# Kernel optimization log

Measured on AMD Instinct MI355X. Metric: run time of the kernel, lower is better.

The kernel has to match this reference:

```python
import jax, jax.numpy as jnp
import numpy as np

PC_RANGE = np.array([-51.2, -51.2, -3.2, 51.2, 51.2, 3.2], dtype=np.float32)
VOXEL = 0.2
T_, Z_, Y_, X_ = 5, 32, 512, 512
N_RAYS = 10000
N_STEPS = 768  # unit-voxel steps, enough to traverse the 512x512 grid diagonally


def setup_inputs() -> dict:
    key = jax.random.key(0)
    k1, k2, k3, k4 = jax.random.split(key, 4)
    grid_feats = jax.random.normal(k1, (1, T_, Z_, Y_, X_), jnp.float32)
    # sensor origins near the ego vehicle (meters)
    output_origin = jax.random.uniform(k2, (1, T_, 3), jnp.float32, -2.0, 2.0)
    # LiDAR endpoints: wide in x/y, shallow in z (meters)
    pts = jax.random.normal(k3, (1, N_RAYS, 3), jnp.float32) * 15.0
    pts = pts.at[..., 2].set(jnp.clip(pts[..., 2] * 0.1, -3.0, 3.0))
    output_tindex = jax.random.randint(k4, (1, N_RAYS), 0, T_, dtype=jnp.int32)
    return {"grid_feats": grid_feats, "output_origin": output_origin,
            "output_points": pts, "output_tindex": output_tindex}


def _render(sigma, origin_v, points_v, tindex):
    """Volumetric ray marching (dvr.render math, fixed-step traversal).
    sigma: [B,T,Z,Y,X] nonneg densities; origin_v/points_v in voxel coords (x,y,z).
    Returns expected termination distance and gt distance per ray (voxel units)."""
    B, T, Z, Y, X = sigma.shape
    tindex = tindex.astype(jnp.int32)
    orig = jnp.take_along_axis(origin_v, tindex[..., None].astype(jnp.int32), axis=1)  # [B,N,3]
    dirv = points_v - orig
    gt_dist = jnp.linalg.norm(dirv, axis=-1)                       # [B,N]
    unit = dirv / jnp.maximum(gt_dist[..., None], 1e-6)
    t = jnp.arange(N_STEPS, dtype=sigma.dtype) + 0.5               # [K] step = 1 voxel
    pos = orig[:, :, None, :] + unit[:, :, None, :] * t[None, None, :, None]  # [B,N,K,3]
    idx = jnp.floor(pos).astype(jnp.int32)
    ix, iy, iz = idx[..., 0], idx[..., 1], idx[..., 2]
    inb = (ix >= 0) & (ix < X) & (iy >= 0) & (iy < Y) & (iz >= 0) & (iz < Z)
    ixc = jnp.clip(ix, 0, X - 1)
    iyc = jnp.clip(iy, 0, Y - 1)
    izc = jnp.clip(iz, 0, Z - 1)
    bidx = jnp.arange(B, dtype=jnp.int32)[:, None, None]
    sig = sigma[bidx, tindex[:, :, None], izc, iyc, ixc]           # [B,N,K]
    tau = jnp.where(inb, sig, 0.0)                                 # dt = 1 voxel
    trans = jnp.exp(-(jnp.cumsum(tau, axis=-1) - tau))             # exclusive transmittance
    w = trans * (1.0 - jnp.exp(-tau))                              # termination prob per step
    pred_dist = jnp.sum(w * t, axis=-1)                            # expected depth [B,N]
    return pred_dist, gt_dist


def reference(grid_feats, output_origin, output_points, output_tindex):
    offset = jnp.asarray(PC_RANGE[:3])
    origin_v = (output_origin - offset) / VOXEL
    points_v = (output_points - offset) / VOXEL
    sigma = jax.nn.relu(grid_feats)
    pred, gt = _render(sigma, origin_v, points_v, output_tindex)
    pred = pred * VOXEL
    gt = gt * VOXEL
    valid = gt >= 0
    count = jnp.maximum(valid.sum(), 1).astype(pred.dtype)
    diff = gt - pred
    l1 = jnp.where(valid, jnp.abs(diff), 0.0).sum() / count
    l2 = jnp.where(valid, diff * diff * 0.5, 0.0).sum() / count
    absrel = jnp.where(valid, jnp.abs(diff) / jnp.maximum(gt, 1e-6), 0.0).sum() / count
    return jnp.stack([l1, l2, absrel])
```

## Files before the change

### kernel.cpp

```cpp
#include <hip/hip_runtime.h>
#include <math.h>

#define T_DIM 5
#define Z_DIM 32
#define Y_DIM 512
#define X_DIM 512
#define N_RAYS 10000
#define N_STEPS 768
#define VOXEL_F 0.2f


__global__ __launch_bounds__(256) void render_rays_kernel(
    const float* __restrict__ grid,
    const float* __restrict__ origin,
    const float* __restrict__ points,
    const int*   __restrict__ tindex,
    float4*      __restrict__ loss4)
{
    const int wid  = (int)((blockIdx.x * blockDim.x + threadIdx.x) >> 6);
    const int lane = (int)(threadIdx.x & 63);
    if (wid >= N_RAYS) return;
    const int ray = wid;

    const int ti = tindex[ray];
    const float ox = (origin[ti * 3 + 0] + 51.2f) * 5.0f;
    const float oy = (origin[ti * 3 + 1] + 51.2f) * 5.0f;
    const float oz = (origin[ti * 3 + 2] + 3.2f) * 5.0f;
    const float px = (points[ray * 3 + 0] + 51.2f) * 5.0f;
    const float py = (points[ray * 3 + 1] + 51.2f) * 5.0f;
    const float pz = (points[ray * 3 + 2] + 3.2f) * 5.0f;

    const float dx = px - ox, dy = py - oy, dz = pz - oz;
    const float gt_vox = sqrtf(dx * dx + dy * dy + dz * dz);
    const float inv = 1.0f / fmaxf(gt_vox, 1e-6f);
    const float ux = dx * inv, uy = dy * inv, uz = dz * inv;

    float thi = 1e30f;
    thi = fminf(thi, fmaxf((0.0f - ox) / ux, ((float)X_DIM - ox) / ux));
    thi = fminf(thi, fmaxf((0.0f - oy) / uy, ((float)Y_DIM - oy) / uy));
    thi = fminf(thi, fmaxf((0.0f - oz) / uz, ((float)Z_DIM - oz) / uz));
    int n_active = (int)ceilf(fminf(thi, 769.0f) - 0.5f);
    n_active = min(N_STEPS, max(0, n_active));
    const int iters = (n_active + 63) >> 6;

    const float* gbase = grid + (size_t)ti * (size_t)(Z_DIM * Y_DIM * X_DIM);

    float lane_acc = 0.0f;
    float ecarry   = 1.0f;

    for (int j = 0; j < iters; ++j) {
        const int step = (j << 6) + lane;
        const float tt = (float)step + 0.5f;
        const int ix = (int)floorf(fmaf(ux, tt, ox));
        const int iy = (int)floorf(fmaf(uy, tt, oy));
        const int iz = (int)floorf(fmaf(uz, tt, oz));
        const bool inb = (ix >= 0) & (ix < X_DIM) & (iy >= 0) & (iy < Y_DIM) &
                         (iz >= 0) & (iz < Z_DIM);
        float tau = 0.0f;
        if ((step < n_active) && inb) {
            tau = fmaxf(gbase[((size_t)iz * Y_DIM + (size_t)iy) * X_DIM + (size_t)ix], 0.0f);
        }

        float scan = tau;
#pragma unroll
        for (int d = 1; d < 64; d <<= 1) {
            const float up = __shfl_up(scan, d, 64);
            if (lane >= d) scan += up;
        }

        const float e_scan = expf(-scan);
        lane_acc += ecarry * (expf(tau - scan) - e_scan) * tt;

        ecarry *= __shfl(e_scan, 63, 64);
        if (ecarry < 1e-7f) break;
    }

#pragma unroll
    for (int d = 32; d >= 1; d >>= 1) lane_acc += __shfl_xor(lane_acc, d, 64);

    if (lane == 0) {
        const float pred_m = lane_acc * VOXEL_F;
        const float gt_m   = gt_vox * VOXEL_F;
        const float diff = gt_m - pred_m;
        const float ad   = fabsf(diff);
        float4 v;
        v.x = ad;
        v.y = 0.5f * diff * diff;
        v.z = ad / fmaxf(gt_m, 1e-6f);
        v.w = 1.0f;
        loss4[wid] = v;
    }
}

__global__ __launch_bounds__(1024) void finalize_kernel(
    const float4* __restrict__ loss4, float* __restrict__ out)
{
    const int tid  = (int)threadIdx.x;
    const int lane = tid & 63;
    const int wv   = tid >> 6;
    float a = 0.0f, b = 0.0f, c = 0.0f, n = 0.0f;
    for (int i = tid; i < N_RAYS; i += 1024) {
        const float4 v = loss4[i];
        a += v.x; b += v.y; c += v.z; n += v.w;
    }
#pragma unroll
    for (int d = 32; d >= 1; d >>= 1) {
        a += __shfl_xor(a, d, 64);
        b += __shfl_xor(b, d, 64);
        c += __shfl_xor(c, d, 64);
        n += __shfl_xor(n, d, 64);
    }
    __shared__ float red[16][4];
    if (lane == 0) { red[wv][0] = a; red[wv][1] = b; red[wv][2] = c; red[wv][3] = n; }
    __syncthreads();
    if (wv == 0 && lane < 16) {
        a = red[lane][0]; b = red[lane][1]; c = red[lane][2]; n = red[lane][3];
#pragma unroll
        for (int d = 8; d >= 1; d >>= 1) {
            a += __shfl_xor(a, d, 64);
            b += __shfl_xor(b, d, 64);
            c += __shfl_xor(c, d, 64);
            n += __shfl_xor(n, d, 64);
        }
        if (lane == 0) {
            const float cnt = fmaxf(n, 1.0f);
            out[0] = a / cnt;
            out[1] = b / cnt;
            out[2] = c / cnt;
        }
    }
}

extern "C" void kernel_launch(void* const* d_in, const int* in_sizes, int n_in,
                              void* d_out, int out_size, void* d_ws, size_t ws_size,
                              hipStream_t stream) {
    const float* grid    = (const float*)d_in[0];
    const float* origin  = (const float*)d_in[1];
    const float* points  = (const float*)d_in[2];
    const int*   tindex  = (const int*)d_in[3];
    float*  out   = (float*)d_out;
    float4* loss4 = (float4*)d_ws;

    const int waves_per_block = 256 / 64;
    const int blocks = (N_RAYS + waves_per_block - 1) / waves_per_block;
    render_rays_kernel<<<blocks, 256, 0, stream>>>(grid, origin, points, tindex, loss4);

    finalize_kernel<<<1, 1024, 0, stream>>>(loss4, out);
}
```

Measured before the change: 209.7 us.

## Use 16-ray blocks with in-block loss reduction and uniform origin selection

New measurement: 205.9 us, median of 2. About the same (-1.8%).

```diff
diff --git a/kernel.cpp b/kernel.cpp
--- a/kernel.cpp
+++ b/kernel.cpp
@@ -8,42 +8,54 @@
 #define N_RAYS 10000
 #define N_STEPS 768
 #define VOXEL_F 0.2f
+#define RAYS_PER_BLOCK 16
+#define N_BLOCKS (N_RAYS / RAYS_PER_BLOCK)
 
 
-__global__ __launch_bounds__(256) void render_rays_kernel(
+__global__ __launch_bounds__(1024) void render_rays_kernel(
     const float* __restrict__ grid,
     const float* __restrict__ origin,
     const float* __restrict__ points,
     const int*   __restrict__ tindex,
-    float4*      __restrict__ loss4)
+    float4*      __restrict__ partials)
 {
-    const int wid  = (int)((blockIdx.x * blockDim.x + threadIdx.x) >> 6);
+    const int wv   = (int)(threadIdx.x >> 6);
     const int lane = (int)(threadIdx.x & 63);
-    if (wid >= N_RAYS) return;
-    const int ray = wid;
+    const int ray  = (int)blockIdx.x * RAYS_PER_BLOCK + wv;
 
-    const int ti = tindex[ray];
-    const float ox = (origin[ti * 3 + 0] + 51.2f) * 5.0f;
-    const float oy = (origin[ti * 3 + 1] + 51.2f) * 5.0f;
-    const float oz = (origin[ti * 3 + 2] + 3.2f) * 5.0f;
+    const int ti = __builtin_amdgcn_readfirstlane(tindex[ray]);
     const float px = (points[ray * 3 + 0] + 51.2f) * 5.0f;
     const float py = (points[ray * 3 + 1] + 51.2f) * 5.0f;
     const float pz = (points[ray * 3 + 2] + 3.2f) * 5.0f;
+    const float o0  = origin[0],  o1  = origin[1],  o2  = origin[2];
+    const float o3  = origin[3],  o4  = origin[4],  o5  = origin[5];
+    const float o6  = origin[6],  o7  = origin[7],  o8  = origin[8];
+    const float o9  = origin[9],  o10 = origin[10], o11 = origin[11];
+    const float o12 = origin[12], o13 = origin[13], o14 = origin[14];
+
+    float oxm = o0, oym = o1, ozm = o2;
+    if (ti == 1) { oxm = o3;  oym = o4;  ozm = o5;  }
+    if (ti == 2) { oxm = o6;  oym = o7;  ozm = o8;  }
+    if (ti == 3) { oxm = o9;  oym = o10; ozm = o11; }
+    if (ti == 4) { oxm = o12; oym = o13; ozm = o14; }
+    const float ox = (oxm + 51.2f) * 5.0f;
+    const float oy = (oym + 51.2f) * 5.0f;
+    const float oz = (ozm + 3.2f) * 5.0f;
 
     const float dx = px - ox, dy = py - oy, dz = pz - oz;
     const float gt_vox = sqrtf(dx * dx + dy * dy + dz * dz);
     const float inv = 1.0f / fmaxf(gt_vox, 1e-6f);
     const float ux = dx * inv, uy = dy * inv, uz = dz * inv;
 
+    const float* gbase = grid + (size_t)ti * (size_t)(Z_DIM * Y_DIM * X_DIM);
+
     float thi = 1e30f;
     thi = fminf(thi, fmaxf((0.0f - ox) / ux, ((float)X_DIM - ox) / ux));
     thi = fminf(thi, fmaxf((0.0f - oy) / uy, ((float)Y_DIM - oy) / uy));
     thi = fminf(thi, fmaxf((0.0f - oz) / uz, ((float)Z_DIM - oz) / uz));
     int n_active = (int)ceilf(fminf(thi, 769.0f) - 0.5f);
-    n_active = min(N_STEPS, max(0, n_active));
+    n_active = min(N_STEPS, max(1, n_active));
     const int iters = (n_active + 63) >> 6;
-
-    const float* gbase = grid + (size_t)ti * (size_t)(Z_DIM * Y_DIM * X_DIM);
 
     float lane_acc = 0.0f;
     float ecarry   = 1.0f;
@@ -57,7 +69,7 @@
         const bool inb = (ix >= 0) & (ix < X_DIM) & (iy >= 0) & (iy < Y_DIM) &
                          (iz >= 0) & (iz < Z_DIM);
         float tau = 0.0f;
-        if ((step < n_active) && inb) {
+        if (inb) {
             tau = fmaxf(gbase[((size_t)iz * Y_DIM + (size_t)iy) * X_DIM + (size_t)ix], 0.0f);
         }
 
@@ -78,6 +90,7 @@
 #pragma unroll
     for (int d = 32; d >= 1; d >>= 1) lane_acc += __shfl_xor(lane_acc, d, 64);
 
+    __shared__ float4 slots[RAYS_PER_BLOCK];
     if (lane == 0) {
         const float pred_m = lane_acc * VOXEL_F;
         const float gt_m   = gt_vox * VOXEL_F;
@@ -87,43 +100,59 @@
         v.x = ad;
         v.y = 0.5f * diff * diff;
         v.z = ad / fmaxf(gt_m, 1e-6f);
-        v.w = 1.0f;
-        loss4[wid] = v;
+        v.w = 0.0f;
+        slots[wv] = v;
+    }
+    __syncthreads();
+    if (wv == 0) {
+        float a = 0.0f, b = 0.0f, c = 0.0f;
+        if (lane < RAYS_PER_BLOCK) {
+            const float4 v = slots[lane];
+            a = v.x; b = v.y; c = v.z;
+        }
+#pragma unroll
+        for (int d = 8; d >= 1; d >>= 1) {
+            a += __shfl_xor(a, d, 64);
+            b += __shfl_xor(b, d, 64);
+            c += __shfl_xor(c, d, 64);
+        }
+        if (lane == 0) {
+            float4 p; p.x = a; p.y = b; p.z = c; p.w = 0.0f;
+            partials[blockIdx.x] = p;
+        }
     }
 }
 
-__global__ __launch_bounds__(1024) void finalize_kernel(
-    const float4* __restrict__ loss4, float* __restrict__ out)
+__global__ __launch_bounds__(256) void finalize_kernel(
+    const float4* __restrict__ partials, float* __restrict__ out)
 {
     const int tid  = (int)threadIdx.x;
     const int lane = tid & 63;
     const int wv   = tid >> 6;
-    float a = 0.0f, b = 0.0f, c = 0.0f, n = 0.0f;
-    for (int i = tid; i < N_RAYS; i += 1024) {
-        const float4 v = loss4[i];
-        a += v.x; b += v.y; c += v.z; n += v.w;
+    float a = 0.0f, b = 0.0f, c = 0.0f;
+    for (int i = tid; i < N_BLOCKS; i += 256) {
+        const float4 v = partials[i];
+        a += v.x; b += v.y; c += v.z;
     }
 #pragma unroll
     for (int d = 32; d >= 1; d >>= 1) {
         a += __shfl_xor(a, d, 64);
         b += __shfl_xor(b, d, 64);
         c += __shfl_xor(c, d, 64);
-        n += __shfl_xor(n, d, 64);
     }
-    __shared__ float red[16][4];
-    if (lane == 0) { red[wv][0] = a; red[wv][1] = b; red[wv][2] = c; red[wv][3] = n; }
+    __shared__ float red[4][3];
+    if (lane == 0) { red[wv][0] = a; red[wv][1] = b; red[wv][2] = c; }
     __syncthreads();
-    if (wv == 0 && lane < 16) {
-        a = red[lane][0]; b = red[lane][1]; c = red[lane][2]; n = red[lane][3];
+    if (wv == 0 && lane < 4) {
+        a = red[lane][0]; b = red[lane][1]; c = red[lane][2];
 #pragma unroll
-        for (int d = 8; d >= 1; d >>= 1) {
+        for (int d = 2; d >= 1; d >>= 1) {
             a += __shfl_xor(a, d, 64);
             b += __shfl_xor(b, d, 64);
             c += __shfl_xor(c, d, 64);
-            n += __shfl_xor(n, d, 64);
         }
         if (lane == 0) {
-            const float cnt = fmaxf(n, 1.0f);
+            const float cnt = (float)N_RAYS;
             out[0] = a / cnt;
             out[1] = b / cnt;
             out[2] = c / cnt;
@@ -138,12 +167,9 @@
     const float* origin  = (const float*)d_in[1];
     const float* points  = (const float*)d_in[2];
     const int*   tindex  = (const int*)d_in[3];
-    float*  out   = (float*)d_out;
-    float4* loss4 = (float4*)d_ws;
+    float*  out      = (float*)d_out;
+    float4* partials = (float4*)d_ws;
 
-    const int waves_per_block = 256 / 64;
-    const int blocks = (N_RAYS + waves_per_block - 1) / waves_per_block;
-    render_rays_kernel<<<blocks, 256, 0, stream>>>(grid, origin, points, tindex, loss4);
-
-    finalize_kernel<<<1, 1024, 0, stream>>>(loss4, out);
+    render_rays_kernel<<<N_BLOCKS, 1024, 0, stream>>>(grid, origin, points, tindex, partials);
+    finalize_kernel<<<1, 256, 0, stream>>>(partials, out);
 }
```
